# Optimization experiments

Hardware: AMD Instinct MI355X
Metric: run time of the kernel (lower is better)

## Reference

```python
import jax, jax.numpy as jnp
import numpy as np

B, S, D = 1, 2048, 128   # batch, seq_len, num_hidden (== head dim)
H, KVH = 32, 8           # num_heads, num_kv_heads
REP = H // KVH           # num_rep = 4
D_K = 128                # softmax scale denominator sqrt(d_k)
ROPE_THETA = 10000.0


def _rope(x):
    # x: (B, h, S, D). Standard rotate-half RoPE over last dim, positions on axis -2.
    inv_freq = 1.0 / (ROPE_THETA ** (jnp.arange(0, D, 2, dtype=jnp.float32) / D))  # (D/2,)
    ang = jnp.arange(S, dtype=jnp.float32)[:, None] * inv_freq                      # (S, D/2)
    cos = jnp.concatenate([jnp.cos(ang), jnp.cos(ang)], axis=-1)                    # (S, D)
    sin = jnp.concatenate([jnp.sin(ang), jnp.sin(ang)], axis=-1)
    x1, x2 = jnp.split(x, 2, axis=-1)
    rot = jnp.concatenate([-x2, x1], axis=-1)
    return x * cos + rot * sin


def setup_inputs() -> dict:
    key = jax.random.key(0)
    ks = jax.random.split(key, 11)
    w = 0.02
    return {
        "query":  jax.random.normal(ks[0], (B, S, D), jnp.float32),
        "keys":   jax.random.normal(ks[1], (B, S, D), jnp.float32),
        "values": jax.random.normal(ks[2], (B, S, D), jnp.float32),
        "Wq": jax.random.normal(ks[3], (D, H * D), jnp.float32) * w,
        "bq": jnp.zeros((H * D,), jnp.float32),
        "Wk": jax.random.normal(ks[4], (D, KVH * D), jnp.float32) * w,
        "bk": jnp.zeros((KVH * D,), jnp.float32),
        "Wv": jax.random.normal(ks[5], (D, KVH * D), jnp.float32) * w,
        "bv": jnp.zeros((KVH * D,), jnp.float32),
        "Wo": jax.random.normal(ks[6], (H * D, D), jnp.float32) * w,
        "bo": jnp.zeros((D,), jnp.float32),
    }


def reference(query, keys, values, Wq, bq, Wk, bk, Wv, bv, Wo, bo):
    # Projections; faithful to torch .view(): plain reshape (B,S,h*D)->(B,h,S,D), no transpose.
    q = (query @ Wq + bq).reshape(B, H, S, D)
    k = (keys @ Wk + bk).reshape(B, KVH, S, D)
    v = (values @ Wv + bv).reshape(B, KVH, S, D)
    k = _rope(k)
    v = _rope(v)  # module applies RoPE to values too
    # torch repeat tiles kv heads: q head i <-> kv head (i % KVH).
    qg = q.reshape(B, REP, KVH, S, D)
    scores = jnp.einsum('brgsd,bgtd->brgst', qg, k) / jnp.sqrt(jnp.float32(D_K))
    attn = jax.nn.softmax(scores, axis=-1)  # mask=False path, no causal mask
    out = jnp.einsum('brgst,bgtd->brgsd', attn, v).reshape(B, H, S, D)
    out = out.transpose(0, 2, 1, 3).reshape(B, S, H * D)
    return out @ Wo + bo
```

## Files before the change

### kernel.cpp

```cpp
#include <hip/hip_runtime.h>
#include <math.h>


#define SCALE 0.08838834764831843f
#define L2_10K_64 0.20762050593045952f

typedef short bf16x8 __attribute__((ext_vector_type(8)));
typedef float f32x4 __attribute__((ext_vector_type(4)));

__device__ __forceinline__ unsigned short f2b(float f) {
  union { float f; unsigned u; } x; x.f = f;
  return (unsigned short)((x.u + 0x7FFFu + ((x.u >> 16) & 1u)) >> 16);
}
__device__ __forceinline__ float b2f(unsigned short b) {
  union { unsigned u; float f; } x; x.u = ((unsigned)b) << 16;
  return x.f;
}
__device__ __forceinline__ void lds_dma16(void* lds, const void* g) {
  __builtin_amdgcn_global_load_lds(
      (const __attribute__((address_space(1))) unsigned int*)g,
      (__attribute__((address_space(3))) unsigned int*)lds, 16, 0, 0);
}

__global__ void prep_weights(const float* __restrict__ Wk, const float* __restrict__ Wv,
                             const float* __restrict__ Wo, const float* __restrict__ Wq,
                             const float* __restrict__ bo,
                             unsigned short* __restrict__ Wkt, unsigned short* __restrict__ Wvt,
                             unsigned short* __restrict__ Wot, unsigned short* __restrict__ Wq2,
                             float* __restrict__ out, int big) {
  int b = blockIdx.x, tid = threadIdx.x;
  if (b < 512) {
    int idx = b * 256 + tid;
    int n = idx >> 7, k = idx & 127;
    Wkt[idx] = f2b(Wk[(size_t)k * 1024 + n]);
  } else if (b < 1024) {
    int idx = (b - 512) * 256 + tid;
    int n = idx >> 7, k = idx & 127;
    Wvt[idx] = f2b(Wv[(size_t)k * 1024 + n]);
  } else if (b < 3072) {
    int idx = (b - 1024) * 256 + tid;
    int n = idx >> 12, k = idx & 4095;
    Wot[idx] = f2b(Wo[(size_t)k * 128 + n]);
  } else if (b < 5120) {
    int idx = (b - 3072) * 256 + tid;
    if (big) {
      int n = idx >> 7, k = idx & 127;
      Wq2[idx] = f2b(Wq[(size_t)k * 4096 + n]);
    } else {
      Wq2[idx] = f2b(Wq[idx]);
    }
  } else {
    int idx = (b - 5120) * 256 + tid;
    out[idx] = bo[idx & 127];
  }
}

__global__ __launch_bounds__(256) void proj_all(
    const float* __restrict__ keys, const float* __restrict__ values,
    const float* __restrict__ query,
    const unsigned short* __restrict__ Wkt, const unsigned short* __restrict__ Wvt,
    const unsigned short* __restrict__ Wqt,
    const float* __restrict__ bk, const float* __restrict__ bv, const float* __restrict__ bq,
    unsigned short* __restrict__ kp, unsigned short* __restrict__ vt,
    unsigned short* __restrict__ qp) {
  int bx = blockIdx.x, m0 = blockIdx.y * 64;
  int tid = threadIdx.x;
  int w = tid >> 6, l = tid & 63;
  int l16 = l & 15, g4 = l >> 4;
  int arow = m0 + w * 16 + l16;
  const f32x4 fz = {0.f, 0.f, 0.f, 0.f};

  if (bx >= 16) {
    int n0 = (bx - 16) * 64;
    f32x4 acc[4];
#pragma unroll
    for (int nb = 0; nb < 4; ++nb) acc[nb] = fz;
#pragma unroll
    for (int kc = 0; kc < 4; ++kc) {
      int kbase = kc * 32 + g4 * 8;
      const float* xp = query + (size_t)arow * 128 + kbase;
      bf16x8 a;
#pragma unroll
      for (int j = 0; j < 8; ++j) a[j] = (short)f2b(xp[j]);
#pragma unroll
      for (int nb = 0; nb < 4; ++nb) {
        bf16x8 b = *(const bf16x8*)(Wqt + (size_t)(n0 + nb * 16 + l16) * 128 + kbase);
        acc[nb] = __builtin_amdgcn_mfma_f32_16x16x32_bf16(a, b, acc[nb], 0, 0, 0);
      }
    }
#pragma unroll
    for (int nb = 0; nb < 4; ++nb) {
      int n = n0 + nb * 16 + l16;
      float bvv = bq[n];
#pragma unroll
      for (int r = 0; r < 4; ++r) {
        int mi = m0 + w * 16 + g4 * 4 + r;
        int h = mi >> 6;
        int s = ((mi & 63) << 5) | (n >> 7);
        int d = n & 127;
        qp[((size_t)h * 2048 + s) * 128 + d] = f2b(acc[nb][r] + bvv);
      }
    }
    return;
  }

  int vmode = bx >> 3;
  int n0 = (bx & 7) * 128, tb = bx & 7;
  const float* X = vmode ? values : keys;
  const unsigned short* Wt = vmode ? Wvt : Wkt;
  const float* bias = vmode ? bv : bk;
  f32x4 acc[8];
#pragma unroll
  for (int nb = 0; nb < 8; ++nb) acc[nb] = fz;
#pragma unroll
  for (int kc = 0; kc < 4; ++kc) {
    int kbase = kc * 32 + g4 * 8;
    const float* xp = X + (size_t)arow * 128 + kbase;
    bf16x8 a;
#pragma unroll
    for (int j = 0; j < 8; ++j) a[j] = (short)f2b(xp[j]);
#pragma unroll
    for (int nb = 0; nb < 8; ++nb) {
      bf16x8 b = *(const bf16x8*)(Wt + (size_t)(n0 + nb * 16 + l16) * 128 + kbase);
      acc[nb] = __builtin_amdgcn_mfma_f32_16x16x32_bf16(a, b, acc[nb], 0, 0, 0);
    }
  }
#pragma unroll
  for (int nb = 0; nb < 4; ++nb) {
    int d2 = nb * 16 + l16;
    float invf = exp2f(-(float)d2 * L2_10K_64);
    float blo = bias[n0 + d2], bhi = bias[n0 + d2 + 64];
#pragma unroll
    for (int r = 0; r < 4; ++r) {
      int mi = m0 + w * 16 + g4 * 4 + r;
      int t = (mi & 255) * 8 + tb;
      float ang = (float)t * invf;
      float sf, cf;
      __sincosf(ang, &sf, &cf);
      float x1 = acc[nb][r] + blo;
      float x2 = acc[nb + 4][r] + bhi;
      unsigned short lo = f2b(x1 * cf - x2 * sf);
      unsigned short hi = f2b(x2 * cf + x1 * sf);
      int g = mi >> 8;
      if (vmode) {
        vt[(size_t)g * 262144 + (size_t)d2 * 2048 + t] = lo;
        vt[(size_t)g * 262144 + (size_t)(d2 + 64) * 2048 + t] = hi;
      } else {
        kp[(size_t)g * 262144 + (size_t)t * 128 + d2] = lo;
        kp[(size_t)g * 262144 + (size_t)t * 128 + d2 + 64] = hi;
      }
    }
  }
}

__global__ void ws_marker(float* __restrict__ out) {
  out[blockIdx.x * 256 + threadIdx.x] = 12345.0f;
}

template <int FUSED_Q>
__global__ __launch_bounds__(256, 2) void attn_kernel(
    const float* __restrict__ X, const unsigned short* __restrict__ Wqb,
    const float* __restrict__ bq, const unsigned short* __restrict__ qp,
    const unsigned short* __restrict__ kp, const unsigned short* __restrict__ vt,
    const unsigned short* __restrict__ Wot, float* __restrict__ out) {
  __shared__ __align__(16) char smem[43008];
  int bid = blockIdx.x;
  int h = bid & 31, g = h & 7;
  int qi0 = (bid >> 5) * 128;
  int tid = threadIdx.x;
  int w = tid >> 6, l = tid & 63;
  int l16 = l & 15, g4 = l >> 4;

  const f32x4 fz = {0.f, 0.f, 0.f, 0.f};
  bf16x8 qfrag[2][4];

  if (FUSED_Q) {
    unsigned short* Uni = (unsigned short*)smem;
    int r0 = h * 64 + (qi0 >> 5);
    int col0 = tid * 16;
#pragma unroll
    for (int jp = 0; jp < 2; ++jp) {
      float acc[2][16];
#pragma unroll
      for (int j = 0; j < 2; ++j)
#pragma unroll
        for (int cc = 0; cc < 16; ++cc) acc[j][cc] = bq[col0 + cc];
      const float* xr0 = X + (size_t)(r0 + jp * 2) * 128;
      const float* xr1 = xr0 + 128;
      for (int k = 0; k < 128; ++k) {
        float x0 = xr0[k], x1 = xr1[k];
        bf16x8 w0 = *(const bf16x8*)(Wqb + (size_t)k * 4096 + col0);
        bf16x8 w1 = *(const bf16x8*)(Wqb + (size_t)k * 4096 + col0 + 8);
#pragma unroll
        for (int e = 0; e < 8; ++e) {
          float f0 = b2f((unsigned short)w0[e]), f1 = b2f((unsigned short)w1[e]);
          acc[0][e] += x0 * f0; acc[0][8 + e] += x0 * f1;
          acc[1][e] += x1 * f0; acc[1][8 + e] += x1 * f1;
        }
      }
#pragma unroll
      for (int j = 0; j < 2; ++j)
#pragma unroll
        for (int cc = 0; cc < 16; ++cc)
          Uni[(jp * 2 + j) * 4096 + col0 + cc] = f2b(acc[j][cc]);
    }
    __syncthreads();
#pragma unroll
    for (int a = 0; a < 2; ++a) {
      int srow = w * 32 + a * 16 + l16;
      int sj = srow >> 5, scol = (srow & 31) * 128;
#pragma unroll
      for (int kc = 0; kc < 4; ++kc)
        qfrag[a][kc] = *(const bf16x8*)&Uni[sj * 4096 + scol + kc * 32 + g4 * 8];
    }
    __syncthreads();
  } else {
#pragma unroll
    for (int a = 0; a < 2; ++a) {
      const unsigned short* qrow =
          qp + ((size_t)h * 2048 + qi0 + w * 32 + a * 16 + l16) * 128;
#pragma unroll
      for (int kc = 0; kc < 4; ++kc)
        qfrag[a][kc] = *(const bf16x8*)(qrow + kc * 32 + g4 * 8);
    }
  }

  const char* kg = (const char*)(kp + (size_t)g * 262144);
  const char* vg = (const char*)(vt + (size_t)g * 262144);
  unsigned short* PsW = (unsigned short*)(smem + 32768) + w * 1280;

#define STAGE_K(tn, kb)                                                          \
  {                                                                              \
    _Pragma("unroll") for (int i = 0; i < 2; ++i) {                              \
      int off = w * 2048 + i * 1024 + l * 16;                                    \
      int row = off >> 8, ch = (off >> 4) & 15;                                  \
      int rch = ch ^ (row & 7);                                                  \
      lds_dma16(smem + (kb) * 8192 + w * 2048 + i * 1024,                        \
                kg + (size_t)(tn) * 8192 + (size_t)row * 256 + rch * 16);        \
    }                                                                            \
  }
#define STAGE_V(tn, vb)                                                          \
  {                                                                              \
    _Pragma("unroll") for (int i = 0; i < 2; ++i) {                              \
      int off = w * 2048 + i * 1024 + l * 16;                                    \
      int vrow = off >> 6, vcb = off & 63;                                       \
      lds_dma16(smem + 16384 + (vb) * 8192 + w * 2048 + i * 1024,                \
                vg + (size_t)vrow * 4096 + (size_t)(tn) * 64 + vcb);             \
    }                                                                            \
  }

  STAGE_K(0, 0);
  STAGE_V(0, 0);
  __syncthreads();

  f32x4 oacc[2][8];
#pragma unroll
  for (int a = 0; a < 2; ++a)
#pragma unroll
    for (int db = 0; db < 8; ++db) oacc[a][db] = fz;
  float lacc[2][4] = {{0.f, 0.f, 0.f, 0.f}, {0.f, 0.f, 0.f, 0.f}};

  int c = 0;
  for (int t = 0; t < 64; ++t) {
    if (t < 63) {
      STAGE_K(t + 1, c ^ 1);
      STAGE_V(t + 1, c ^ 1);
    }

    f32x4 sacc[2][2];
    sacc[0][0] = fz; sacc[0][1] = fz; sacc[1][0] = fz; sacc[1][1] = fz;
    __builtin_amdgcn_s_setprio(1);
#pragma unroll
    for (int kc = 0; kc < 4; ++kc) {
#pragma unroll
      for (int jb = 0; jb < 2; ++jb) {
        int krow = jb * 16 + l16;
        int rch = (kc * 4 + g4) ^ (krow & 7);
        bf16x8 bfrag = *(const bf16x8*)(smem + c * 8192 + krow * 256 + rch * 16);
        sacc[0][jb] = __builtin_amdgcn_mfma_f32_16x16x32_bf16(qfrag[0][kc], bfrag, sacc[0][jb], 0, 0, 0);
        sacc[1][jb] = __builtin_amdgcn_mfma_f32_16x16x32_bf16(qfrag[1][kc], bfrag, sacc[1][jb], 0, 0, 0);
      }
    }
    __builtin_amdgcn_s_setprio(0);
#pragma unroll
    for (int a = 0; a < 2; ++a) {
#pragma unroll
      for (int r = 0; r < 4; ++r) {
        unsigned short u0 = f2b(__expf(sacc[a][0][r] * SCALE));
        unsigned short u1 = f2b(__expf(sacc[a][1][r] * SCALE));
        lacc[a][r] += b2f(u0) + b2f(u1);
        PsW[(a * 16 + g4 * 4 + r) * 40 + l16] = u0;
        PsW[(a * 16 + g4 * 4 + r) * 40 + 16 + l16] = u1;
      }
    }
    bf16x8 pfrag0 = *(const bf16x8*)(PsW + (l16)*40 + g4 * 8);
    bf16x8 pfrag1 = *(const bf16x8*)(PsW + (16 + l16) * 40 + g4 * 8);
    __builtin_amdgcn_s_setprio(1);
#pragma unroll
    for (int db = 0; db < 8; ++db) {
      bf16x8 vfrag = *(const bf16x8*)(smem + 16384 + c * 8192 + (db * 16 + l16) * 64 + g4 * 16);
      oacc[0][db] = __builtin_amdgcn_mfma_f32_16x16x32_bf16(pfrag0, vfrag, oacc[0][db], 0, 0, 0);
      oacc[1][db] = __builtin_amdgcn_mfma_f32_16x16x32_bf16(pfrag1, vfrag, oacc[1][db], 0, 0, 0);
    }
    __builtin_amdgcn_s_setprio(0);
    __syncthreads();
    c ^= 1;
  }

  float invl[2][4];
#pragma unroll
  for (int a = 0; a < 2; ++a)
#pragma unroll
    for (int r = 0; r < 4; ++r) {
      float v = lacc[a][r];
#pragma unroll
      for (int off = 1; off < 16; off <<= 1) v += __shfl_xor(v, off, 64);
      invl[a][r] = 1.f / v;
    }

  unsigned short* Otile = (unsigned short*)smem;
#pragma unroll
  for (int a = 0; a < 2; ++a)
#pragma unroll
    for (int db = 0; db < 8; ++db)
#pragma unroll
      for (int r = 0; r < 4; ++r)
        Otile[(w * 32 + a * 16 + g4 * 4 + r) * 136 + db * 16 + l16] =
            f2b(oacc[a][db][r] * invl[a][r]);
  __syncthreads();
  bf16x8 a2[2][4];
#pragma unroll
  for (int a = 0; a < 2; ++a)
#pragma unroll
    for (int kc = 0; kc < 4; ++kc)
      a2[a][kc] = *(const bf16x8*)&Otile[(w * 32 + a * 16 + l16) * 136 + kc * 32 + g4 * 8];
  f32x4 acc2[2][8];
#pragma unroll
  for (int a = 0; a < 2; ++a)
#pragma unroll
    for (int nb = 0; nb < 8; ++nb) acc2[a][nb] = fz;
#pragma unroll
  for (int kc = 0; kc < 4; ++kc) {
#pragma unroll
    for (int nb = 0; nb < 8; ++nb) {
      bf16x8 b2v = *(const bf16x8*)(Wot + (size_t)(nb * 16 + l16) * 4096 + h * 128 + kc * 32 + g4 * 8);
      acc2[0][nb] = __builtin_amdgcn_mfma_f32_16x16x32_bf16(a2[0][kc], b2v, acc2[0][nb], 0, 0, 0);
      acc2[1][nb] = __builtin_amdgcn_mfma_f32_16x16x32_bf16(a2[1][kc], b2v, acc2[1][nb], 0, 0, 0);
    }
  }
#pragma unroll
  for (int a = 0; a < 2; ++a)
#pragma unroll
    for (int nb = 0; nb < 8; ++nb)
#pragma unroll
      for (int r = 0; r < 4; ++r)
        atomicAdd(&out[(size_t)(qi0 + w * 32 + a * 16 + g4 * 4 + r) * 128 + nb * 16 + l16],
                  acc2[a][nb][r]);
#undef STAGE_K
#undef STAGE_V
}

extern "C" void kernel_launch(void* const* d_in, const int* in_sizes, int n_in,
                              void* d_out, int out_size, void* d_ws, size_t ws_size,
                              hipStream_t stream) {
  const float* query  = (const float*)d_in[0];
  const float* keys   = (const float*)d_in[1];
  const float* values = (const float*)d_in[2];
  const float* Wq = (const float*)d_in[3];
  const float* bq = (const float*)d_in[4];
  const float* Wk = (const float*)d_in[5];
  const float* bk = (const float*)d_in[6];
  const float* Wv = (const float*)d_in[7];
  const float* bv = (const float*)d_in[8];
  const float* Wo = (const float*)d_in[9];
  const float* bo = (const float*)d_in[10];
  float* out = (float*)d_out;
  char* ws = (char*)d_ws;
  const size_t MB = 1024 * 1024;
  if (ws_size < 10 * MB + 512 * 1024) {
    ws_marker<<<1024, 256, 0, stream>>>(out);
    return;
  }
  unsigned short* Wq2   = (unsigned short*)(ws);
  unsigned short* Wkt   = (unsigned short*)(ws + 1 * MB);
  unsigned short* Wvt   = (unsigned short*)(ws + 1 * MB + 256 * 1024);
  unsigned short* Wot   = (unsigned short*)(ws + 1 * MB + 512 * 1024);
  unsigned short* kproj = (unsigned short*)(ws + 2 * MB + 512 * 1024);
  unsigned short* vt    = (unsigned short*)(ws + 6 * MB + 512 * 1024);
  unsigned short* qproj = (unsigned short*)(ws + 10 * MB + 512 * 1024);
  int big = ws_size >= 27 * MB;

  prep_weights<<<6144, 256, 0, stream>>>(Wk, Wv, Wo, Wq, bo, Wkt, Wvt, Wot, Wq2, out, big);

  if (big) {
    proj_all<<<dim3(80, 32), 256, 0, stream>>>(keys, values, query, Wkt, Wvt, Wq2,
                                               bk, bv, bq, kproj, vt, qproj);
    attn_kernel<0><<<512, 256, 0, stream>>>(query, Wq2, bq, qproj, kproj, vt, Wot, out);
  } else {
    proj_all<<<dim3(16, 32), 256, 0, stream>>>(keys, values, query, Wkt, Wvt, Wq2,
                                               bk, bv, bq, kproj, vt, qproj);
    attn_kernel<1><<<512, 256, 0, stream>>>(query, Wq2, bq, nullptr, kproj, vt, Wot, out);
  }
}
```

Before: 173.2 us.

## Triple-buffer K/V tiles with vmcnt waits and tile-transpose weight prep

The attention loop moves from double to triple buffering of K/V tiles in LDS, prefetching two tiles ahead and replacing the full __syncthreads with an explicit vmcnt wait plus a raw barrier, so global-to-LDS DMA overlaps with compute. The weight-prep kernel now transposes through a shared-memory 64x64 tile, giving coalesced reads and writes, and runs far fewer blocks. The softmax exponent switches to exp2f with a folded log2(e) scale. The larger LDS footprint (about 58 KB) may cut occupancy below the two blocks per CU the launch bounds ask for, and the hand-written vmcnt counts must match the number of outstanding DMA loads.

Result: slower. 182.2 us (+5.2%).

```diff
diff --git a/kernel.cpp b/kernel.cpp
--- a/kernel.cpp
+++ b/kernel.cpp
@@ -3,6 +3,7 @@
 
 
 #define SCALE 0.08838834764831843f
+#define SCALE_L2E 0.12751878222550723f
 #define L2_10K_64 0.20762050593045952f
 
 typedef short bf16x8 __attribute__((ext_vector_type(8)));
@@ -22,36 +23,50 @@
       (__attribute__((address_space(3))) unsigned int*)lds, 16, 0, 0);
 }
 
-__global__ void prep_weights(const float* __restrict__ Wk, const float* __restrict__ Wv,
-                             const float* __restrict__ Wo, const float* __restrict__ Wq,
-                             const float* __restrict__ bo,
-                             unsigned short* __restrict__ Wkt, unsigned short* __restrict__ Wvt,
-                             unsigned short* __restrict__ Wot, unsigned short* __restrict__ Wq2,
-                             float* __restrict__ out, int big) {
+__global__ __launch_bounds__(256) void prep_weights(
+    const float* __restrict__ Wk, const float* __restrict__ Wv,
+    const float* __restrict__ Wo, const float* __restrict__ Wq,
+    const float* __restrict__ bo,
+    unsigned short* __restrict__ Wkt, unsigned short* __restrict__ Wvt,
+    unsigned short* __restrict__ Wot, unsigned short* __restrict__ Wq2,
+    float* __restrict__ out, int big) {
+  __shared__ unsigned short T[64][66];
   int b = blockIdx.x, tid = threadIdx.x;
-  if (b < 512) {
-    int idx = b * 256 + tid;
-    int n = idx >> 7, k = idx & 127;
-    Wkt[idx] = f2b(Wk[(size_t)k * 1024 + n]);
-  } else if (b < 1024) {
-    int idx = (b - 512) * 256 + tid;
-    int n = idx >> 7, k = idx & 127;
-    Wvt[idx] = f2b(Wv[(size_t)k * 1024 + n]);
-  } else if (b < 3072) {
-    int idx = (b - 1024) * 256 + tid;
-    int n = idx >> 12, k = idx & 4095;
-    Wot[idx] = f2b(Wo[(size_t)k * 128 + n]);
-  } else if (b < 5120) {
-    int idx = (b - 3072) * 256 + tid;
-    if (big) {
-      int n = idx >> 7, k = idx & 127;
-      Wq2[idx] = f2b(Wq[(size_t)k * 4096 + n]);
-    } else {
-      Wq2[idx] = f2b(Wq[idx]);
-    }
+  const float* W;
+  unsigned short* D;
+  int K, N, tk, tn;
+  if (b < 32) {
+    W = Wk; D = Wkt; K = 128; N = 1024; int ti = b;       tk = ti & 1;  tn = ti >> 1;
+  } else if (b < 64) {
+    W = Wv; D = Wvt; K = 128; N = 1024; int ti = b - 32;  tk = ti & 1;  tn = ti >> 1;
+  } else if (b < 192) {
+    W = Wo; D = Wot; K = 4096; N = 128; int ti = b - 64;  tk = ti >> 1; tn = ti & 1;
+  } else if (b < 320) {
+    if (!big) {
+      int i0 = ((b - 192) * 256 + tid) * 16;
+#pragma unroll
+      for (int j = 0; j < 16; ++j) Wq2[i0 + j] = f2b(Wq[i0 + j]);
+      return;
+    }
+    W = Wq; D = Wq2; K = 128; N = 4096; int ti = b - 192; tk = ti & 1;  tn = ti >> 1;
   } else {
-    int idx = (b - 5120) * 256 + tid;
-    out[idx] = bo[idx & 127];
+    int i0 = ((b - 320) * 256 + tid) * 16;
+#pragma unroll
+    for (int j = 0; j < 16; ++j) out[i0 + j] = bo[(i0 + j) & 127];
+    return;
+  }
+  int k0 = tk * 64, n0 = tn * 64;
+  int c = tid & 63, q = tid >> 6;
+#pragma unroll
+  for (int i = 0; i < 16; ++i) {
+    int r = i * 4 + q;
+    T[r][c] = f2b(W[(size_t)(k0 + r) * N + n0 + c]);
+  }
+  __syncthreads();
+#pragma unroll
+  for (int i = 0; i < 16; ++i) {
+    int r = i * 4 + q;
+    D[(size_t)(n0 + r) * K + k0 + c] = T[c][r];
   }
 }
 
@@ -97,8 +112,7 @@
         int mi = m0 + w * 16 + g4 * 4 + r;
         int h = mi >> 6;
         int s = ((mi & 63) << 5) | (n >> 7);
-        int d = n & 127;
-        qp[((size_t)h * 2048 + s) * 128 + d] = f2b(acc[nb][r] + bvv);
+        qp[((size_t)h * 2048 + s) * 128 + (n & 127)] = f2b(acc[nb][r] + bvv);
       }
     }
     return;
@@ -163,7 +177,7 @@
     const float* __restrict__ bq, const unsigned short* __restrict__ qp,
     const unsigned short* __restrict__ kp, const unsigned short* __restrict__ vt,
     const unsigned short* __restrict__ Wot, float* __restrict__ out) {
-  __shared__ __align__(16) char smem[43008];
+  __shared__ __align__(16) char smem[59392];
   int bid = blockIdx.x;
   int h = bid & 31, g = h & 7;
   int qi0 = (bid >> 5) * 128;
@@ -227,7 +241,7 @@
 
   const char* kg = (const char*)(kp + (size_t)g * 262144);
   const char* vg = (const char*)(vt + (size_t)g * 262144);
-  unsigned short* PsW = (unsigned short*)(smem + 32768) + w * 1280;
+  unsigned short* PsW = (unsigned short*)(smem + 49152) + w * 1280;
 
 #define STAGE_K(tn, kb)                                                          \
   {                                                                              \
@@ -244,13 +258,13 @@
     _Pragma("unroll") for (int i = 0; i < 2; ++i) {                              \
       int off = w * 2048 + i * 1024 + l * 16;                                    \
       int vrow = off >> 6, vcb = off & 63;                                       \
-      lds_dma16(smem + 16384 + (vb) * 8192 + w * 2048 + i * 1024,                \
+      lds_dma16(smem + 24576 + (vb) * 8192 + w * 2048 + i * 1024,                \
                 vg + (size_t)vrow * 4096 + (size_t)(tn) * 64 + vcb);             \
     }                                                                            \
   }
 
-  STAGE_K(0, 0);
-  STAGE_V(0, 0);
+  STAGE_K(0, 0); STAGE_V(0, 0);
+  STAGE_K(1, 1); STAGE_V(1, 1);
   __syncthreads();
 
   f32x4 oacc[2][8];
@@ -260,11 +274,12 @@
     for (int db = 0; db < 8; ++db) oacc[a][db] = fz;
   float lacc[2][4] = {{0.f, 0.f, 0.f, 0.f}, {0.f, 0.f, 0.f, 0.f}};
 
-  int c = 0;
   for (int t = 0; t < 64; ++t) {
-    if (t < 63) {
-      STAGE_K(t + 1, c ^ 1);
-      STAGE_V(t + 1, c ^ 1);
+    int cb = t % 3;
+    if (t < 62) {
+      int nb3 = (t + 2) % 3;
+      STAGE_K(t + 2, nb3);
+      STAGE_V(t + 2, nb3);
     }
 
     f32x4 sacc[2][2];
@@ -276,7 +291,7 @@
       for (int jb = 0; jb < 2; ++jb) {
         int krow = jb * 16 + l16;
         int rch = (kc * 4 + g4) ^ (krow & 7);
-        bf16x8 bfrag = *(const bf16x8*)(smem + c * 8192 + krow * 256 + rch * 16);
+        bf16x8 bfrag = *(const bf16x8*)(smem + cb * 8192 + krow * 256 + rch * 16);
         sacc[0][jb] = __builtin_amdgcn_mfma_f32_16x16x32_bf16(qfrag[0][kc], bfrag, sacc[0][jb], 0, 0, 0);
         sacc[1][jb] = __builtin_amdgcn_mfma_f32_16x16x32_bf16(qfrag[1][kc], bfrag, sacc[1][jb], 0, 0, 0);
       }
@@ -286,25 +301,30 @@
     for (int a = 0; a < 2; ++a) {
 #pragma unroll
       for (int r = 0; r < 4; ++r) {
-        unsigned short u0 = f2b(__expf(sacc[a][0][r] * SCALE));
-        unsigned short u1 = f2b(__expf(sacc[a][1][r] * SCALE));
+        unsigned short u0 = f2b(exp2f(sacc[a][0][r] * SCALE_L2E));
+        unsigned short u1 = f2b(exp2f(sacc[a][1][r] * SCALE_L2E));
         lacc[a][r] += b2f(u0) + b2f(u1);
         PsW[(a * 16 + g4 * 4 + r) * 40 + l16] = u0;
         PsW[(a * 16 + g4 * 4 + r) * 40 + 16 + l16] = u1;
       }
     }
-    bf16x8 pfrag0 = *(const bf16x8*)(PsW + (l16)*40 + g4 * 8);
+    bf16x8 pfrag0 = *(const bf16x8*)(PsW + l16 * 40 + g4 * 8);
     bf16x8 pfrag1 = *(const bf16x8*)(PsW + (16 + l16) * 40 + g4 * 8);
     __builtin_amdgcn_s_setprio(1);
 #pragma unroll
     for (int db = 0; db < 8; ++db) {
-      bf16x8 vfrag = *(const bf16x8*)(smem + 16384 + c * 8192 + (db * 16 + l16) * 64 + g4 * 16);
+      bf16x8 vfrag = *(const bf16x8*)(smem + 24576 + cb * 8192 + (db * 16 + l16) * 64 + g4 * 16);
       oacc[0][db] = __builtin_amdgcn_mfma_f32_16x16x32_bf16(pfrag0, vfrag, oacc[0][db], 0, 0, 0);
       oacc[1][db] = __builtin_amdgcn_mfma_f32_16x16x32_bf16(pfrag1, vfrag, oacc[1][db], 0, 0, 0);
     }
     __builtin_amdgcn_s_setprio(0);
-    __syncthreads();
-    c ^= 1;
+
+    if (t < 63) {
+      if (t < 62) asm volatile("s_waitcnt vmcnt(4)" ::: "memory");
+      else        asm volatile("s_waitcnt vmcnt(0)" ::: "memory");
+      __builtin_amdgcn_s_barrier();
+      __builtin_amdgcn_sched_barrier(0);
+    }
   }
 
   float invl[2][4];
@@ -318,6 +338,7 @@
       invl[a][r] = 1.f / v;
     }
 
+  __syncthreads();
   unsigned short* Otile = (unsigned short*)smem;
 #pragma unroll
   for (int a = 0; a < 2; ++a)
@@ -390,7 +411,7 @@
   unsigned short* qproj = (unsigned short*)(ws + 10 * MB + 512 * 1024);
   int big = ws_size >= 27 * MB;
 
-  prep_weights<<<6144, 256, 0, stream>>>(Wk, Wv, Wo, Wq, bo, Wkt, Wvt, Wot, Wq2, out, big);
+  prep_weights<<<384, 256, 0, stream>>>(Wk, Wv, Wo, Wq, bo, Wkt, Wvt, Wot, Wq2, out, big);
 
   if (big) {
     proj_all<<<dim3(80, 32), 256, 0, stream>>>(keys, values, query, Wkt, Wvt, Wq2,
```
